# Kernel tuning notes

Hardware: AMD Instinct MI355X
Metric: run time of the kernel (lower is better)

Reference implementation:

```python
import jax, jax.numpy as jnp
import numpy as np

EMBED_DIM = 384
NUM_HEADS = 6
HEAD_DIM = EMBED_DIM // NUM_HEADS
SCALE = HEAD_DIM ** -0.5


def setup_inputs() -> dict:
    key = jax.random.key(0)
    k1, k2 = jax.random.split(key)
    b, n, q, hw, c = 8, 5, 15, 196, EMBED_DIM
    k = 5  # shots
    x_query = jax.random.normal(k1, (b, n, q, hw, c), dtype=jnp.float32)
    x_support = jax.random.normal(k2, (b, n, k, c), dtype=jnp.float32)
    return {"x_query": x_query, "x_support": x_support}


def reference(x_query, x_support):
    b, n, k, c = x_support.shape
    _, _, q, hw, _ = x_query.shape
    h, d = NUM_HEADS, HEAD_DIM
    M = n * k            # support tokens
    P = n * q            # query images
    # support tokens as per-head queries: (b, M, h, d)
    qs = x_support.reshape(b, M, h, d)
    # query patch tokens as per-head keys/values: (b, P, hw, h, d)
    kv = x_query.reshape(b, P, hw, h, d)
    # broadcast single support-query block across all P key/value blocks
    # attn: (b, P, h, M, hw)
    attn = jnp.einsum('bmhd,bpwhd->bphmw', qs, kv) * SCALE
    attn = jax.nn.softmax(attn, axis=-1)
    # o: (b, P, M, h, d) -> (b, P, M, c)
    o_query = jnp.einsum('bphmw,bpwhd->bpmhd', attn, kv).reshape(b, P, M, c)
    o_support = x_support.reshape(b, 1, M, c)
    return (o_query, o_support)
```

## Files before the change

### kernel.cpp

```cpp
#include <hip/hip_runtime.h>
#include <stdint.h>

#define HW   196
#define CC   384
#define HH   6
#define DD   64
#define MM   25
#define PP   75
#define BB   8
#define NT   512

#define KVW  35
#define KTW  115
#define SCW  113

#define OQ_SIZE (BB * PP * MM * CC)

typedef float  f32x4 __attribute__((ext_vector_type(4)));
typedef short  s16x8 __attribute__((ext_vector_type(8)));
union Frag { uint32_t u[4]; s16x8 v; };

__device__ __forceinline__ float bflo(uint32_t u) { return __uint_as_float(u << 16); }
__device__ __forceinline__ float bfhi(uint32_t u) { return __uint_as_float(u & 0xffff0000u); }
__device__ __forceinline__ uint16_t f2bf(float f) {
    uint32_t u = __float_as_uint(f);
    u += 0x7fffu + ((u >> 16) & 1);
    return (uint16_t)(u >> 16);
}
__device__ __forceinline__ uint32_t pack2bf(float a, float b) {
    return (uint32_t)f2bf(a) | ((uint32_t)f2bf(b) << 16);
}

__global__ __launch_bounds__(NT) void attn_kernel(
    const float* __restrict__ xq,
    const float* __restrict__ xs,
    float* __restrict__ out,
    float* __restrict__ out_sup)
{
    __shared__ union {
        uint32_t kv[208 * KVW];
        uint32_t kvT[64 * KTW];
    } U;
    __shared__ uint32_t scb[32 * SCW];

    const int bid  = blockIdx.x;
    const int h    = bid % HH;
    const int bp   = bid / HH;
    const int b    = bp / PP;
    const int tid  = threadIdx.x;
    const int lane = tid & 63;
    const int wv   = tid >> 6;
    const int lm   = lane & 15;
    const int quad = lane >> 4;

    if (bid < 600 && tid < 16) {
        int idx = bid * 16 + tid;
        ((float4*)out_sup)[idx * 2]     = ((const float4*)xs)[idx * 2];
        ((float4*)out_sup)[idx * 2 + 1] = ((const float4*)xs)[idx * 2 + 1];
    }

    Frag afr[2][2];
    #pragma unroll
    for (int mt = 0; mt < 2; mt++) {
        int row = 16 * mt + lm;
        #pragma unroll
        for (int ks = 0; ks < 2; ks++) {
            if (row < MM) {
                const float* p = xs + (size_t)b * (MM * CC) + row * CC + h * DD + ks * 32 + quad * 8;
                float4 v0 = *(const float4*)p;
                float4 v1 = *(const float4*)(p + 4);
                afr[mt][ks].u[0] = pack2bf(v0.x * 0.125f, v0.y * 0.125f);
                afr[mt][ks].u[1] = pack2bf(v0.z * 0.125f, v0.w * 0.125f);
                afr[mt][ks].u[2] = pack2bf(v1.x * 0.125f, v1.y * 0.125f);
                afr[mt][ks].u[3] = pack2bf(v1.z * 0.125f, v1.w * 0.125f);
            } else {
                afr[mt][ks].u[0] = afr[mt][ks].u[1] = afr[mt][ks].u[2] = afr[mt][ks].u[3] = 0;
            }
        }
    }

    {
        const float* src = xq + (size_t)bp * (HW * CC) + h * DD;
        for (int i = tid; i < HW * 16; i += NT) {
            int w = i >> 4, seg = i & 15;
            float4 v = *(const float4*)(src + (size_t)w * CC + seg * 4);
            U.kv[w * KVW + seg * 2]     = pack2bf(v.x, v.y);
            U.kv[w * KVW + seg * 2 + 1] = pack2bf(v.z, v.w);
        }
        for (int i = tid; i < 12 * 32; i += NT) {
            U.kv[(196 + (i >> 5)) * KVW + (i & 31)] = 0;
        }
    }
    __syncthreads();

    uint32_t tr[16];
    const int tp  = tid >> 2;
    const int tdc = tid & 3;
    if (tid < 416) {
        #pragma unroll
        for (int c = 0; c < 16; c++) {
            int r = c >> 3, cc = c & 7;
            tr[c] = U.kv[(2 * tp + r) * KVW + tdc * 8 + cc];
        }
    }

    {
        uint16_t* scbh = (uint16_t*)scb;
        for (int nt = wv; nt < 13; nt += 8) {
            f32x4 acc0 = {0.f, 0.f, 0.f, 0.f};
            f32x4 acc1 = {0.f, 0.f, 0.f, 0.f};
            #pragma unroll
            for (int ks = 0; ks < 2; ks++) {
                Frag bf;
                int base = (16 * nt + lm) * KVW + ks * 16 + quad * 4;
                bf.u[0] = U.kv[base + 0];
                bf.u[1] = U.kv[base + 1];
                bf.u[2] = U.kv[base + 2];
                bf.u[3] = U.kv[base + 3];
                acc0 = __builtin_amdgcn_mfma_f32_16x16x32_bf16(afr[0][ks].v, bf.v, acc0, 0, 0, 0);
                acc1 = __builtin_amdgcn_mfma_f32_16x16x32_bf16(afr[1][ks].v, bf.v, acc1, 0, 0, 0);
            }
            int wcol = 16 * nt + lm;
            #pragma unroll
            for (int i = 0; i < 4; i++) {
                scbh[(quad * 4 + i) * (2 * SCW) + wcol]        = f2bf(acc0[i]);
                scbh[(16 + quad * 4 + i) * (2 * SCW) + wcol]   = f2bf(acc1[i]);
            }
        }
    }
    __syncthreads();

    for (int m = wv; m < MM; m += 8) {
        uint32_t* row = scb + m * SCW;
        uint32_t u0 = row[lane];
        uint32_t u1 = (lane < 34) ? row[64 + lane] : 0;
        float f0 = bflo(u0), f1 = bfhi(u0);
        float f2 = (lane < 34) ? bflo(u1) : -1e30f;
        float f3 = (lane < 34) ? bfhi(u1) : -1e30f;
        float mx = fmaxf(fmaxf(f0, f1), fmaxf(f2, f3));
        #pragma unroll
        for (int off = 32; off > 0; off >>= 1) mx = fmaxf(mx, __shfl_xor(mx, off, 64));
        float e0 = __expf(f0 - mx), e1 = __expf(f1 - mx);
        float e2 = (lane < 34) ? __expf(f2 - mx) : 0.f;
        float e3 = (lane < 34) ? __expf(f3 - mx) : 0.f;
        float s = e0 + e1 + e2 + e3;
        #pragma unroll
        for (int off = 32; off > 0; off >>= 1) s += __shfl_xor(s, off, 64);
        float inv = 1.0f / s;
        row[lane] = pack2bf(e0 * inv, e1 * inv);
        if (lane < 34)      row[64 + lane] = pack2bf(e2 * inv, e3 * inv);
        else if (lane < 48) row[64 + lane] = 0;
    }
    __syncthreads();

    if (tid < 416) {
        #pragma unroll
        for (int c = 0; c < 16; c++) {
            int d = 16 * tdc + c;
            uint32_t e0 = (tr[c >> 1]     >> (16 * (c & 1))) & 0xffffu;
            uint32_t e1 = (tr[8 + (c >> 1)] >> (16 * (c & 1))) & 0xffffu;
            U.kvT[d * KTW + tp] = e0 | (e1 << 16);
        }
    } else {
        for (int i = tid - 416; i < 64 * 8; i += 96)
            U.kvT[(i >> 3) * KTW + 104 + (i & 7)] = 0;
    }
    __syncthreads();

    {
        const int mt  = wv >> 2;
        const int nt2 = wv & 3;
        f32x4 acc = {0.f, 0.f, 0.f, 0.f};
        #pragma unroll
        for (int ks = 0; ks < 7; ks++) {
            Frag a, bf;
            int abase = (16 * mt + lm) * SCW + ks * 16 + quad * 4;
            a.u[0] = scb[abase + 0];
            a.u[1] = scb[abase + 1];
            a.u[2] = scb[abase + 2];
            a.u[3] = scb[abase + 3];
            int bbase = (16 * nt2 + lm) * KTW + ks * 16 + quad * 4;
            bf.u[0] = U.kvT[bbase + 0];
            bf.u[1] = U.kvT[bbase + 1];
            bf.u[2] = U.kvT[bbase + 2];
            bf.u[3] = U.kvT[bbase + 3];
            acc = __builtin_amdgcn_mfma_f32_16x16x32_bf16(a.v, bf.v, acc, 0, 0, 0);
        }
        float* ob = out + (size_t)bp * (MM * CC) + h * DD + 16 * nt2 + lm;
        #pragma unroll
        for (int i = 0; i < 4; i++) {
            int m = 16 * mt + quad * 4 + i;
            if (m < MM) ob[(size_t)m * CC] = acc[i];
        }
    }
}

extern "C" void kernel_launch(void* const* d_in, const int* in_sizes, int n_in,
                              void* d_out, int out_size, void* d_ws, size_t ws_size,
                              hipStream_t stream) {
    const float* xq = (const float*)d_in[0];
    const float* xs = (const float*)d_in[1];
    float* out = (float*)d_out;
    float* out_sup = out + (size_t)OQ_SIZE;
    attn_kernel<<<BB * PP * HH, NT, 0, stream>>>(xq, xs, out, out_sup);
}
```

Measured before the change: 275.2 us.

## Load K fragments directly from global and write transposed V to LDS

```diff
diff --git a/kernel.cpp b/kernel.cpp
--- a/kernel.cpp
+++ b/kernel.cpp
@@ -10,8 +10,7 @@
 #define BB   8
 #define NT   512
 
-#define KVW  35
-#define KTW  115
+#define KTW  113
 #define SCW  113
 
 #define OQ_SIZE (BB * PP * MM * CC)
@@ -22,26 +21,23 @@
 
 __device__ __forceinline__ float bflo(uint32_t u) { return __uint_as_float(u << 16); }
 __device__ __forceinline__ float bfhi(uint32_t u) { return __uint_as_float(u & 0xffff0000u); }
-__device__ __forceinline__ uint16_t f2bf(float f) {
-    uint32_t u = __float_as_uint(f);
-    u += 0x7fffu + ((u >> 16) & 1);
-    return (uint16_t)(u >> 16);
+__device__ __forceinline__ uint32_t pk_bf16(float a, float b) {
+    union { __bf16 h[2]; uint32_t u; } r;
+    r.h[0] = (__bf16)a; r.h[1] = (__bf16)b;
+    return r.u;
 }
-__device__ __forceinline__ uint32_t pack2bf(float a, float b) {
-    return (uint32_t)f2bf(a) | ((uint32_t)f2bf(b) << 16);
+__device__ __forceinline__ uint16_t bf16_1(float a) {
+    union { __bf16 h; uint16_t u; } r; r.h = (__bf16)a; return r.u;
 }
 
-__global__ __launch_bounds__(NT) void attn_kernel(
+__global__ __launch_bounds__(NT, 6) void attn_kernel(
     const float* __restrict__ xq,
     const float* __restrict__ xs,
     float* __restrict__ out,
     float* __restrict__ out_sup)
 {
-    __shared__ union {
-        uint32_t kv[208 * KVW];
-        uint32_t kvT[64 * KTW];
-    } U;
-    __shared__ uint32_t scb[32 * SCW];
+    __shared__ uint32_t kvT[64 * KTW];
+    __shared__ uint32_t scb[MM * SCW];
 
     const int bid  = blockIdx.x;
     const int h    = bid % HH;
@@ -59,6 +55,8 @@
         ((float4*)out_sup)[idx * 2 + 1] = ((const float4*)xs)[idx * 2 + 1];
     }
 
+    kvT[(tid >> 3) * KTW + 104 + (tid & 7)] = 0;
+
     Frag afr[2][2];
     #pragma unroll
     for (int mt = 0; mt < 2; mt++) {
@@ -69,10 +67,10 @@
                 const float* p = xs + (size_t)b * (MM * CC) + row * CC + h * DD + ks * 32 + quad * 8;
                 float4 v0 = *(const float4*)p;
                 float4 v1 = *(const float4*)(p + 4);
-                afr[mt][ks].u[0] = pack2bf(v0.x * 0.125f, v0.y * 0.125f);
-                afr[mt][ks].u[1] = pack2bf(v0.z * 0.125f, v0.w * 0.125f);
-                afr[mt][ks].u[2] = pack2bf(v1.x * 0.125f, v1.y * 0.125f);
-                afr[mt][ks].u[3] = pack2bf(v1.z * 0.125f, v1.w * 0.125f);
+                afr[mt][ks].u[0] = pk_bf16(v0.x * 0.125f, v0.y * 0.125f);
+                afr[mt][ks].u[1] = pk_bf16(v0.z * 0.125f, v0.w * 0.125f);
+                afr[mt][ks].u[2] = pk_bf16(v1.x * 0.125f, v1.y * 0.125f);
+                afr[mt][ks].u[3] = pk_bf16(v1.z * 0.125f, v1.w * 0.125f);
             } else {
                 afr[mt][ks].u[0] = afr[mt][ks].u[1] = afr[mt][ks].u[2] = afr[mt][ks].u[3] = 0;
             }
@@ -80,51 +78,55 @@
     }
 
     {
-        const float* src = xq + (size_t)bp * (HW * CC) + h * DD;
-        for (int i = tid; i < HW * 16; i += NT) {
-            int w = i >> 4, seg = i & 15;
-            float4 v = *(const float4*)(src + (size_t)w * CC + seg * 4);
-            U.kv[w * KVW + seg * 2]     = pack2bf(v.x, v.y);
-            U.kv[w * KVW + seg * 2 + 1] = pack2bf(v.z, v.w);
-        }
-        for (int i = tid; i < 12 * 32; i += NT) {
-            U.kv[(196 + (i >> 5)) * KVW + (i & 31)] = 0;
-        }
-    }
-    __syncthreads();
-
-    uint32_t tr[16];
-    const int tp  = tid >> 2;
-    const int tdc = tid & 3;
-    if (tid < 416) {
-        #pragma unroll
-        for (int c = 0; c < 16; c++) {
-            int r = c >> 3, cc = c & 7;
-            tr[c] = U.kv[(2 * tp + r) * KVW + tdc * 8 + cc];
-        }
-    }
-
-    {
         uint16_t* scbh = (uint16_t*)scb;
+        uint16_t* kvh  = (uint16_t*)kvT;
+        const float* slab = xq + (size_t)bp * (HW * CC) + h * DD;
         for (int nt = wv; nt < 13; nt += 8) {
+            const int w = 16 * nt + lm;
+            float4 v[2][2];
+            if (w < HW) {
+                const float* p = slab + (size_t)w * CC + quad * 8;
+                #pragma unroll
+                for (int ks = 0; ks < 2; ks++) {
+                    v[ks][0] = *(const float4*)(p + ks * 32);
+                    v[ks][1] = *(const float4*)(p + ks * 32 + 4);
+                }
+            } else {
+                #pragma unroll
+                for (int ks = 0; ks < 2; ks++) {
+                    v[ks][0].x = v[ks][0].y = v[ks][0].z = v[ks][0].w = 0.f;
+                    v[ks][1].x = v[ks][1].y = v[ks][1].z = v[ks][1].w = 0.f;
+                }
+            }
+            Frag bf[2];
+            #pragma unroll
+            for (int ks = 0; ks < 2; ks++) {
+                bf[ks].u[0] = pk_bf16(v[ks][0].x, v[ks][0].y);
+                bf[ks].u[1] = pk_bf16(v[ks][0].z, v[ks][0].w);
+                bf[ks].u[2] = pk_bf16(v[ks][1].x, v[ks][1].y);
+                bf[ks].u[3] = pk_bf16(v[ks][1].z, v[ks][1].w);
+            }
             f32x4 acc0 = {0.f, 0.f, 0.f, 0.f};
             f32x4 acc1 = {0.f, 0.f, 0.f, 0.f};
             #pragma unroll
             for (int ks = 0; ks < 2; ks++) {
-                Frag bf;
-                int base = (16 * nt + lm) * KVW + ks * 16 + quad * 4;
-                bf.u[0] = U.kv[base + 0];
-                bf.u[1] = U.kv[base + 1];
-                bf.u[2] = U.kv[base + 2];
-                bf.u[3] = U.kv[base + 3];
-                acc0 = __builtin_amdgcn_mfma_f32_16x16x32_bf16(afr[0][ks].v, bf.v, acc0, 0, 0, 0);
-                acc1 = __builtin_amdgcn_mfma_f32_16x16x32_bf16(afr[1][ks].v, bf.v, acc1, 0, 0, 0);
+                acc0 = __builtin_amdgcn_mfma_f32_16x16x32_bf16(afr[0][ks].v, bf[ks].v, acc0, 0, 0, 0);
+                acc1 = __builtin_amdgcn_mfma_f32_16x16x32_bf16(afr[1][ks].v, bf[ks].v, acc1, 0, 0, 0);
             }
-            int wcol = 16 * nt + lm;
+            #pragma unroll
+            for (int ks = 0; ks < 2; ks++) {
+                #pragma unroll
+                for (int c = 0; c < 4; c++) {
+                    int d = 32 * ks + 8 * quad + 2 * c;
+                    kvh[d * (2 * KTW) + w]       = (uint16_t)(bf[ks].u[c] & 0xffffu);
+                    kvh[(d + 1) * (2 * KTW) + w] = (uint16_t)(bf[ks].u[c] >> 16);
+                }
+            }
             #pragma unroll
             for (int i = 0; i < 4; i++) {
-                scbh[(quad * 4 + i) * (2 * SCW) + wcol]        = f2bf(acc0[i]);
-                scbh[(16 + quad * 4 + i) * (2 * SCW) + wcol]   = f2bf(acc1[i]);
+                scbh[(quad * 4 + i) * (2 * SCW) + w] = bf16_1(acc0[i]);
+                int r1 = 16 + quad * 4 + i;
+                if (r1 < MM) scbh[r1 * (2 * SCW) + w] = bf16_1(acc1[i]);
             }
         }
     }
@@ -147,44 +149,32 @@
         #pragma unroll
         for (int off = 32; off > 0; off >>= 1) s += __shfl_xor(s, off, 64);
         float inv = 1.0f / s;
-        row[lane] = pack2bf(e0 * inv, e1 * inv);
-        if (lane < 34)      row[64 + lane] = pack2bf(e2 * inv, e3 * inv);
+        row[lane] = pk_bf16(e0 * inv, e1 * inv);
+        if (lane < 34)      row[64 + lane] = pk_bf16(e2 * inv, e3 * inv);
         else if (lane < 48) row[64 + lane] = 0;
-    }
-    __syncthreads();
-
-    if (tid < 416) {
-        #pragma unroll
-        for (int c = 0; c < 16; c++) {
-            int d = 16 * tdc + c;
-            uint32_t e0 = (tr[c >> 1]     >> (16 * (c & 1))) & 0xffffu;
-            uint32_t e1 = (tr[8 + (c >> 1)] >> (16 * (c & 1))) & 0xffffu;
-            U.kvT[d * KTW + tp] = e0 | (e1 << 16);
-        }
-    } else {
-        for (int i = tid - 416; i < 64 * 8; i += 96)
-            U.kvT[(i >> 3) * KTW + 104 + (i & 7)] = 0;
     }
     __syncthreads();
 
     {
         const int mt  = wv >> 2;
         const int nt2 = wv & 3;
+        int arow = 16 * mt + lm;
+        if (arow >= MM) arow = MM - 1;
         f32x4 acc = {0.f, 0.f, 0.f, 0.f};
         #pragma unroll
         for (int ks = 0; ks < 7; ks++) {
-            Frag a, bf;
-            int abase = (16 * mt + lm) * SCW + ks * 16 + quad * 4;
+            Frag a, bfr;
+            int abase = arow * SCW + ks * 16 + quad * 4;
             a.u[0] = scb[abase + 0];
             a.u[1] = scb[abase + 1];
             a.u[2] = scb[abase + 2];
             a.u[3] = scb[abase + 3];
             int bbase = (16 * nt2 + lm) * KTW + ks * 16 + quad * 4;
-            bf.u[0] = U.kvT[bbase + 0];
-            bf.u[1] = U.kvT[bbase + 1];
-            bf.u[2] = U.kvT[bbase + 2];
-            bf.u[3] = U.kvT[bbase + 3];
-            acc = __builtin_amdgcn_mfma_f32_16x16x32_bf16(a.v, bf.v, acc, 0, 0, 0);
+            bfr.u[0] = kvT[bbase + 0];
+            bfr.u[1] = kvT[bbase + 1];
+            bfr.u[2] = kvT[bbase + 2];
+            bfr.u[3] = kvT[bbase + 3];
+            acc = __builtin_amdgcn_mfma_f32_16x16x32_bf16(a.v, bfr.v, acc, 0, 0, 0);
         }
         float* ob = out + (size_t)bp * (MM * CC) + h * DD + 16 * nt2 + lm;
         #pragma unroll
```

Result: faster. 262.1 us (-4.8%).
